# Kernel optimization log

Measured on AMD Instinct MI355X. Metric: run time of the kernel, lower is better.

Reference implementation:

```python
import jax, jax.numpy as jnp
import numpy as np

N_NODES = 50000


def setup_inputs() -> dict:
    key = jax.random.key(0)
    ks = jax.random.split(key, 8)
    x = jax.random.normal(ks[0], (N_NODES, 128), dtype=jnp.float32)
    edge_index = jax.random.randint(ks[1], (2, 800000), 0, N_NODES, dtype=jnp.int64)
    # Glorot-ish small init for weights
    W1l = jax.random.normal(ks[2], (128, 256), dtype=jnp.float32) * 0.05
    W1r = jax.random.normal(ks[3], (128, 256), dtype=jnp.float32) * 0.05
    b1 = jnp.zeros((256,), dtype=jnp.float32)
    W2l = jax.random.normal(ks[4], (256, 64), dtype=jnp.float32) * 0.05
    W2r = jax.random.normal(ks[5], (256, 64), dtype=jnp.float32) * 0.05
    b2 = jnp.zeros((64,), dtype=jnp.float32)
    return {"x": x, "edge_index": edge_index, "W1l": W1l, "W1r": W1r,
            "b1": b1, "W2l": W2l, "W2r": W2r, "b2": b2}


def _mean_aggregate(x, src, dst, num_nodes):
    # gather neighbor features [E, d], scatter-sum to targets, divide by in-degree
    summed = jax.ops.segment_sum(x[src], dst, num_segments=num_nodes)
    deg = jax.ops.segment_sum(jnp.ones_like(dst, dtype=x.dtype), dst,
                              num_segments=num_nodes)
    return summed / jnp.maximum(deg, 1.0)[:, None]


def _sage_conv(x, src, dst, W_l, W_r, b):
    # PyG SAGEConv (mean aggr): lin_l(mean_j x_j) + lin_r(x); bias only in lin_l
    agg = _mean_aggregate(x, src, dst, x.shape[0])
    return agg @ W_l + b + x @ W_r


def reference(x, edge_index, W1l, W1r, b1, W2l, W2r, b2):
    src, dst = edge_index[0], edge_index[1]
    h = jax.nn.relu(_sage_conv(x, src, dst, W1l, W1r, b1))
    # dropout p=0.5 is identity in eval mode
    out = _sage_conv(h, src, dst, W2l, W2r, b2)
    return out
```

## Files before the change

kernel.cpp:

```cpp
#include <hip/hip_runtime.h>
#include <hip/hip_bf16.h>

#define N_NODES 50000
#define CAP 64
#define NPART 8
#define PSZ 6250

typedef __attribute__((ext_vector_type(8))) __bf16 bf16x8;
typedef __attribute__((ext_vector_type(4))) float f32x4;

__device__ __forceinline__ unsigned short f2bf(float f) {
    union { float f; unsigned u; } c{f};
    unsigned u = c.u;
    return (unsigned short)((u + 0x7FFFu + ((u >> 16) & 1u)) >> 16);
}
__device__ __forceinline__ float bf2f(unsigned h) {
    union { unsigned u; float f; } c{h << 16};
    return c.f;
}
__device__ __forceinline__ unsigned pack2(float a, float b) {
    return (unsigned)f2bf(a) | ((unsigned)f2bf(b) << 16);
}

__device__ __forceinline__ unsigned q8(float v) {
    int q = __float2int_rn(v * 16.0f);
    q = max(-127, min(127, q));
    return (unsigned)(q + 128) & 0xFFu;
}

__global__ __launch_bounds__(256) void zero_kernel(uint4* __restrict__ p, int n4) {
    int i = blockIdx.x * 256 + threadIdx.x;
    if (i < n4) p[i] = (uint4){0u, 0u, 0u, 0u};
}

__global__ __launch_bounds__(256) void prep_all_kernel(
        const int* __restrict__ src, const int* __restrict__ dst,
        int* __restrict__ cnt, int* __restrict__ eidx, int E,
        const float4* __restrict__ x4, uint4* __restrict__ xb4,
        uint2* __restrict__ xq2, int NX,
        const float* __restrict__ W1l, const float* __restrict__ W1r,
        const float* __restrict__ W2l, const float* __restrict__ W2r,
        unsigned short* __restrict__ Wb1l, unsigned short* __restrict__ Wb1r,
        unsigned short* __restrict__ Wb2) {
    const int HB = (E + 1023) / 1024;
    const int CB = (NX + 255) / 256;
    int b = blockIdx.x;
    if (b < HB * NPART) {
        const int part = b & (NPART - 1);
        const int slice = b >> 3;
        const int lo = part * PSZ;
        int base = slice * 1024 + threadIdx.x;
#pragma unroll
        for (int k = 0; k < 4; ++k) {
            int e = base + k * 256;
            if (e < E) {
                int d = dst[e];
                if ((unsigned)(d - lo) < (unsigned)PSZ) {
                    int r = atomicAdd(&cnt[d], 1);
                    eidx[(size_t)d * CAP + (r & (CAP - 1))] = src[e];
                }
            }
        }
        return;
    }
    b -= HB * NPART;
    if (b < CB) {
        int t = b * 256 + threadIdx.x;
        if (t < NX) {
            float4 v0 = x4[2 * t];
            float4 v1 = x4[2 * t + 1];
            uint4 o;
            o.x = pack2(v0.x, v0.y);
            o.y = pack2(v0.z, v0.w);
            o.z = pack2(v1.x, v1.y);
            o.w = pack2(v1.z, v1.w);
            xb4[t] = o;
            uint2 q;
            q.x = q8(v0.x) | (q8(v0.y) << 8) | (q8(v0.z) << 16) | (q8(v0.w) << 24);
            q.y = q8(v1.x) | (q8(v1.y) << 8) | (q8(v1.z) << 16) | (q8(v1.w) << 24);
            xq2[t] = q;
        }
        return;
    }
    b -= CB;
    int t = b * 256 + threadIdx.x;
    if (t >= 12288) return;
    int g = t & 4095;
    int colin = g & 15;
    int rest = g >> 4;
    if (t < 4096) {
        int kb = rest & 15, cb = rest >> 4;
        int col = cb * 16 + colin;
#pragma unroll
        for (int j = 0; j < 8; ++j) Wb1l[g * 8 + j] = f2bf(W1l[(kb * 8 + j) * 256 + col]);
    } else if (t < 8192) {
        int kb = rest & 15, cb = rest >> 4;
        int col = cb * 16 + colin;
#pragma unroll
        for (int j = 0; j < 8; ++j) Wb1r[g * 8 + j] = f2bf(W1r[(kb * 8 + j) * 256 + col]);
    } else {
        int kb = rest & 31, cb = rest >> 5;
        const float* W = (cb < 4) ? W2l : W2r;
        int col = (cb < 4) ? (cb * 16 + colin) : ((cb - 4) * 16 + colin);
#pragma unroll
        for (int j = 0; j < 8; ++j) Wb2[g * 8 + j] = f2bf(W[(kb * 8 + j) * 64 + col]);
    }
}

__global__ __launch_bounds__(256) void agg1_kernel(const uint4* __restrict__ xq4,
        const int* __restrict__ cnt, const int* __restrict__ eidx,
        uint4* __restrict__ aggb4, int N) {
    int t = blockIdx.x * 256 + threadIdx.x;
    int n = t >> 6, lane = t & 63;
    if (n >= N) return;
    int deg = min(cnt[n], CAP);
    const int* el = eidx + (size_t)n * CAP;
    int g = lane >> 3, c = lane & 7;
    float s[16];
#pragma unroll
    for (int k = 0; k < 16; ++k) s[k] = 0.0f;
    for (int j = g; j < deg; j += 8) {
        int idx = el[j];
        uint4 v = xq4[(size_t)idx * 8 + c];
        unsigned w0 = v.x, w1 = v.y, w2 = v.z, w3 = v.w;
#pragma unroll
        for (int byte = 0; byte < 4; ++byte) {
            s[0 + byte]  += (float)((w0 >> (8 * byte)) & 0xFFu);
            s[4 + byte]  += (float)((w1 >> (8 * byte)) & 0xFFu);
            s[8 + byte]  += (float)((w2 >> (8 * byte)) & 0xFFu);
            s[12 + byte] += (float)((w3 >> (8 * byte)) & 0xFFu);
        }
    }
#pragma unroll
    for (int m = 8; m <= 32; m <<= 1) {
#pragma unroll
        for (int k = 0; k < 16; ++k) s[k] += __shfl_xor(s[k], m);
    }
    if (g == 0) {
        float scale = 0.0625f / (float)max(deg, 1);
        float bias = 128.0f * (float)deg;
        float v[16];
#pragma unroll
        for (int k = 0; k < 16; ++k) v[k] = (s[k] - bias) * scale;
        uint4 o0, o1;
        o0.x = pack2(v[0], v[1]);
        o0.y = pack2(v[2], v[3]);
        o0.z = pack2(v[4], v[5]);
        o0.w = pack2(v[6], v[7]);
        o1.x = pack2(v[8], v[9]);
        o1.y = pack2(v[10], v[11]);
        o1.z = pack2(v[12], v[13]);
        o1.w = pack2(v[14], v[15]);
        aggb4[(size_t)n * 16 + c * 2] = o0;
        aggb4[(size_t)n * 16 + c * 2 + 1] = o1;
    }
}

__global__ __launch_bounds__(256, 4) void gemm1_mfma(
        const unsigned short* __restrict__ xb, const unsigned short* __restrict__ aggb,
        const unsigned short* __restrict__ Wb1l, const unsigned short* __restrict__ Wb1r,
        const float* __restrict__ b1, unsigned short* __restrict__ hb, int M) {
    __shared__ uint4 wlds[2048];
    const int tid = threadIdx.x;
    const int wave = tid >> 6, lane = tid & 63;
    const int l16 = lane & 15, lq = lane >> 4;
    const int cg = blockIdx.y;
    const int base_row = blockIdx.x * 256 + wave * 64;
    int row_a[4];
#pragma unroll
    for (int rt = 0; rt < 4; ++rt) row_a[rt] = min(base_row + rt * 16 + l16, M - 1);

    const uint4* Wg1 = reinterpret_cast<const uint4*>(Wb1l) + cg * 1024;
    const uint4* Wg2 = reinterpret_cast<const uint4*>(Wb1r) + cg * 1024;
    for (int i = tid; i < 1024; i += 256) {
        wlds[i] = Wg1[i];
        wlds[1024 + i] = Wg2[i];
    }

    f32x4 acc[4][4];
#pragma unroll
    for (int rt = 0; rt < 4; ++rt)
#pragma unroll
        for (int q = 0; q < 4; ++q) acc[rt][q] = (f32x4){0.f, 0.f, 0.f, 0.f};

    __syncthreads();
#pragma unroll
    for (int s = 0; s < 2; ++s) {
        const unsigned short* A = (s == 0) ? aggb : xb;
        const uint4* wl = wlds + s * 1024;
#pragma unroll
        for (int ks = 0; ks < 4; ++ks) {
            bf16x8 a[4];
#pragma unroll
            for (int rt = 0; rt < 4; ++rt)
                a[rt] = *reinterpret_cast<const bf16x8*>(A + (size_t)row_a[rt] * 128 + ks * 32 + lq * 8);
            int wb = (ks * 4 + lq) * 16 + l16;
#pragma unroll
            for (int q = 0; q < 4; ++q) {
                bf16x8 bfr = *reinterpret_cast<const bf16x8*>(&wl[q * 256 + wb]);
#pragma unroll
                for (int rt = 0; rt < 4; ++rt)
                    acc[rt][q] = __builtin_amdgcn_mfma_f32_16x16x32_bf16(a[rt], bfr, acc[rt][q], 0, 0, 0);
            }
        }
    }

#pragma unroll
    for (int q = 0; q < 4; ++q) {
        int col = (cg * 4 + q) * 16 + l16;
        float bias = b1[col];
#pragma unroll
        for (int rt = 0; rt < 4; ++rt)
#pragma unroll
            for (int r = 0; r < 4; ++r) {
                int row = base_row + rt * 16 + lq * 4 + r;
                if (row < M) {
                    float v = acc[rt][q][r] + bias;
                    hb[(size_t)row * 256 + col] = f2bf(v > 0.0f ? v : 0.0f);
                }
            }
    }
}

__global__ __launch_bounds__(256, 4) void gemm2_mfma(
        const unsigned short* __restrict__ hb, const unsigned short* __restrict__ Wb2,
        unsigned short* __restrict__ tb, float* __restrict__ u, int M) {
    __shared__ uint4 wlds[2048];
    const int tid = threadIdx.x;
    const int wave = tid >> 6, lane = tid & 63;
    const int l16 = lane & 15, lq = lane >> 4;
    const int cg = blockIdx.y;
    const int base_row = blockIdx.x * 256 + wave * 64;
    int row_a[4];
#pragma unroll
    for (int rt = 0; rt < 4; ++rt) row_a[rt] = min(base_row + rt * 16 + l16, M - 1);

    const uint4* Wg = reinterpret_cast<const uint4*>(Wb2) + cg * 2048;
    for (int i = tid; i < 2048; i += 256) wlds[i] = Wg[i];

    f32x4 acc[4][4];
#pragma unroll
    for (int rt = 0; rt < 4; ++rt)
#pragma unroll
        for (int q = 0; q < 4; ++q) acc[rt][q] = (f32x4){0.f, 0.f, 0.f, 0.f};

    __syncthreads();
#pragma unroll
    for (int ks = 0; ks < 8; ++ks) {
        bf16x8 a[4];
#pragma unroll
        for (int rt = 0; rt < 4; ++rt)
            a[rt] = *reinterpret_cast<const bf16x8*>(hb + (size_t)row_a[rt] * 256 + ks * 32 + lq * 8);
        int wb = (ks * 4 + lq) * 16 + l16;
#pragma unroll
        for (int q = 0; q < 4; ++q) {
            bf16x8 bfr = *reinterpret_cast<const bf16x8*>(&wlds[q * 512 + wb]);
#pragma unroll
            for (int rt = 0; rt < 4; ++rt)
                acc[rt][q] = __builtin_amdgcn_mfma_f32_16x16x32_bf16(a[rt], bfr, acc[rt][q], 0, 0, 0);
        }
    }

#pragma unroll
    for (int q = 0; q < 4; ++q) {
        int cb = cg * 4 + q;
#pragma unroll
        for (int rt = 0; rt < 4; ++rt)
#pragma unroll
            for (int r = 0; r < 4; ++r) {
                int row = base_row + rt * 16 + lq * 4 + r;
                if (row >= M) continue;
                float v = acc[rt][q][r];
                if (cb < 4) tb[(size_t)row * 64 + cb * 16 + l16] = f2bf(v);
                else        u[(size_t)row * 64 + (cb - 4) * 16 + l16] = v;
            }
    }
}

__global__ __launch_bounds__(256) void agg2_kernel(const uint4* __restrict__ tb4,
        const float4* __restrict__ u4, const float4* __restrict__ b24,
        const int* __restrict__ cnt, const int* __restrict__ eidx,
        float4* __restrict__ out4, int N) {
    int t = blockIdx.x * 256 + threadIdx.x;
    int n = t >> 6, lane = t & 63;
    if (n >= N) return;
    int deg = min(cnt[n], CAP);
    const int* el = eidx + (size_t)n * CAP;
    int g = lane >> 3, c = lane & 7;
    float s0 = 0, s1 = 0, s2 = 0, s3 = 0, s4 = 0, s5 = 0, s6 = 0, s7 = 0;
    for (int j = g; j < deg; j += 8) {
        int idx = el[j];
        uint4 v = tb4[(size_t)idx * 8 + c];
        s0 += bf2f(v.x & 0xFFFF); s1 += bf2f(v.x >> 16);
        s2 += bf2f(v.y & 0xFFFF); s3 += bf2f(v.y >> 16);
        s4 += bf2f(v.z & 0xFFFF); s5 += bf2f(v.z >> 16);
        s6 += bf2f(v.w & 0xFFFF); s7 += bf2f(v.w >> 16);
    }
#pragma unroll
    for (int m = 8; m <= 32; m <<= 1) {
        s0 += __shfl_xor(s0, m); s1 += __shfl_xor(s1, m);
        s2 += __shfl_xor(s2, m); s3 += __shfl_xor(s3, m);
        s4 += __shfl_xor(s4, m); s5 += __shfl_xor(s5, m);
        s6 += __shfl_xor(s6, m); s7 += __shfl_xor(s7, m);
    }
    if (g == 0) {
        float rd = 1.0f / (float)max(deg, 1);
        float4 ua = u4[(size_t)n * 16 + c * 2];
        float4 ub = u4[(size_t)n * 16 + c * 2 + 1];
        float4 ba = b24[c * 2];
        float4 bb = b24[c * 2 + 1];
        float4 oa = {s0 * rd + ua.x + ba.x, s1 * rd + ua.y + ba.y,
                     s2 * rd + ua.z + ba.z, s3 * rd + ua.w + ba.w};
        float4 ob = {s4 * rd + ub.x + bb.x, s5 * rd + ub.y + bb.y,
                     s6 * rd + ub.z + bb.z, s7 * rd + ub.w + bb.w};
        out4[(size_t)n * 16 + c * 2] = oa;
        out4[(size_t)n * 16 + c * 2 + 1] = ob;
    }
}

extern "C" void kernel_launch(void* const* d_in, const int* in_sizes, int n_in,
                              void* d_out, int out_size, void* d_ws, size_t ws_size,
                              hipStream_t stream) {
    const float* x   = (const float*)d_in[0];
    const int*   ei  = (const int*)d_in[1];
    const float* W1l = (const float*)d_in[2];
    const float* W1r = (const float*)d_in[3];
    const float* b1  = (const float*)d_in[4];
    const float* W2l = (const float*)d_in[5];
    const float* W2r = (const float*)d_in[6];
    const float* b2  = (const float*)d_in[7];
    float* out = (float*)d_out;

    const int E = in_sizes[1] / 2;
    const int N = N_NODES;
    const int* src = ei;
    const int* dst = ei + E;
    const int HB = (E + 1023) / 1024;
    const int NX = N * 16;
    const int CB = (NX + 255) / 256;
    const int WB = 48;

    char* ws = (char*)d_ws;
    int* cnt  = (int*)(ws);
    int* eidx = (int*)(ws + 200000);
    size_t off = 200000 + (size_t)N * CAP * 4;
    off = (off + 15) & ~(size_t)15;
    unsigned short* xb   = (unsigned short*)(ws + off);  off += (size_t)N * 128 * 2;
    unsigned char*  xq   = (unsigned char*)(ws + off);   off += (size_t)N * 128;
    unsigned short* aggb = (unsigned short*)(ws + off);  off += (size_t)N * 128 * 2;
    unsigned short* hb   = (unsigned short*)(ws + off);  off += (size_t)N * 256 * 2;
    unsigned short* tb   = (unsigned short*)(ws + off);  off += (size_t)N * 64 * 2;
    float*          ubuf = (float*)(ws + off);           off += (size_t)N * 64 * 4;
    unsigned short* Wb1l = (unsigned short*)(ws + off);  off += 128 * 256 * 2;
    unsigned short* Wb1r = (unsigned short*)(ws + off);  off += 128 * 256 * 2;
    unsigned short* Wb2  = (unsigned short*)(ws + off);  off += 256 * 128 * 2;

    {
        int n4 = N / 4;
        zero_kernel<<<(n4 + 255) / 256, 256, 0, stream>>>((uint4*)cnt, n4);
    }

    prep_all_kernel<<<HB * NPART + CB + WB, 256, 0, stream>>>(
        src, dst, cnt, eidx, E, (const float4*)x, (uint4*)xb, (uint2*)xq, NX,
        W1l, W1r, W2l, W2r, Wb1l, Wb1r, Wb2);

    agg1_kernel<<<(N * 64 + 255) / 256, 256, 0, stream>>>((const uint4*)xq, cnt, eidx,
                                                          (uint4*)aggb, N);
    {
        dim3 grid((N + 255) / 256, 4);
        gemm1_mfma<<<grid, 256, 0, stream>>>(xb, aggb, Wb1l, Wb1r, b1, hb, N);
    }

    {
        dim3 grid((N + 255) / 256, 2);
        gemm2_mfma<<<grid, 256, 0, stream>>>(hb, Wb2, tb, ubuf, N);
    }
    agg2_kernel<<<(N * 64 + 255) / 256, 256, 0, stream>>>((const uint4*)tb, (const float4*)ubuf,
                                                          (const float4*)b2, cnt, eidx,
                                                          (float4*)out, N);
}
```

Measured before the change: 158.7 us.

## Fuse all stages into one cooperative persistent kernel with grid syncs

Replaces the six separate launches (zero, prep, agg1, gemm1, gemm2, agg2) with one cooperative kernel. It runs each stage as a grid-stride loop over virtual blocks, separated by grid.sync(). The grid is sized from the occupancy query and capped at 1024 blocks. This aims to remove per-launch overhead and inter-kernel gaps, at the cost of grid-wide barriers, fewer resident blocks for the memory-bound gather stages, and repeated LDS weight reloads per tile. The old multi-kernel path remains as a fallback if the cooperative launch fails.

```diff
diff --git a/kernel.cpp b/kernel.cpp
--- a/kernel.cpp
+++ b/kernel.cpp
@@ -1,5 +1,8 @@
 #include <hip/hip_runtime.h>
 #include <hip/hip_bf16.h>
+#include <hip/hip_cooperative_groups.h>
+
+namespace cg = cooperative_groups;
 
 #define N_NODES 50000
 #define CAP 64
@@ -21,11 +24,309 @@
 __device__ __forceinline__ unsigned pack2(float a, float b) {
     return (unsigned)f2bf(a) | ((unsigned)f2bf(b) << 16);
 }
-
-__device__ __forceinline__ unsigned q8(float v) {
+__device__ __forceinline__ unsigned q8x(float v) {
     int q = __float2int_rn(v * 16.0f);
     q = max(-127, min(127, q));
     return (unsigned)(q + 128) & 0xFFu;
+}
+
+struct Prm {
+    const int* src; const int* dst;
+    int* cnt; int* eidx; int E;
+    const float4* x4; uint4* xb4; uint2* xq2; int NX;
+    const float* W1l; const float* W1r; const float* W2l; const float* W2r;
+    unsigned short* Wb1l; unsigned short* Wb1r; unsigned short* Wb2;
+    const float* b1; unsigned short* hb;
+    unsigned short* tb; float* ubuf;
+    const float4* b24; float4* out4;
+    unsigned short* aggb;
+};
+
+__global__ __launch_bounds__(256, 4) void fused_kernel(Prm p) {
+    cg::grid_group grid = cg::this_grid();
+    __shared__ uint4 wlds[2048];
+    const int tid = threadIdx.x;
+    const int bid = blockIdx.x;
+    const int gsz = gridDim.x;
+
+    for (int i = bid * 256 + tid; i < N_NODES / 4; i += gsz * 256)
+        reinterpret_cast<uint4*>(p.cnt)[i] = (uint4){0u, 0u, 0u, 0u};
+    grid.sync();
+
+    {
+        const int HB = (p.E + 1023) / 1024;
+        const int HBP = HB * NPART;
+        const int CB = (p.NX + 255) / 256;
+        const int TOT = HBP + CB + 48;
+        for (int vb = bid; vb < TOT; vb += gsz) {
+            int b = vb;
+            if (b < HBP) {
+                const int part = b & (NPART - 1);
+                const int slice = b >> 3;
+                const int lo = part * PSZ;
+                int base = slice * 1024 + tid;
+#pragma unroll
+                for (int k = 0; k < 4; ++k) {
+                    int e = base + k * 256;
+                    if (e < p.E) {
+                        int d = p.dst[e];
+                        if ((unsigned)(d - lo) < (unsigned)PSZ) {
+                            int r = atomicAdd(&p.cnt[d], 1);
+                            p.eidx[(size_t)d * CAP + (r & (CAP - 1))] = p.src[e];
+                        }
+                    }
+                }
+                continue;
+            }
+            b -= HBP;
+            if (b < CB) {
+                int t = b * 256 + tid;
+                if (t < p.NX) {
+                    float4 v0 = p.x4[2 * t];
+                    float4 v1 = p.x4[2 * t + 1];
+                    uint4 o;
+                    o.x = pack2(v0.x, v0.y);
+                    o.y = pack2(v0.z, v0.w);
+                    o.z = pack2(v1.x, v1.y);
+                    o.w = pack2(v1.z, v1.w);
+                    p.xb4[t] = o;
+                    uint2 q;
+                    q.x = q8x(v0.x) | (q8x(v0.y) << 8) | (q8x(v0.z) << 16) | (q8x(v0.w) << 24);
+                    q.y = q8x(v1.x) | (q8x(v1.y) << 8) | (q8x(v1.z) << 16) | (q8x(v1.w) << 24);
+                    p.xq2[t] = q;
+                }
+                continue;
+            }
+            b -= CB;
+            int t = b * 256 + tid;
+            if (t >= 12288) continue;
+            int g = t & 4095;
+            int colin = g & 15;
+            int rest = g >> 4;
+            if (t < 4096) {
+                int kb = rest & 15, cb = rest >> 4;
+                int col = cb * 16 + colin;
+#pragma unroll
+                for (int j = 0; j < 8; ++j) p.Wb1l[g * 8 + j] = f2bf(p.W1l[(kb * 8 + j) * 256 + col]);
+            } else if (t < 8192) {
+                int kb = rest & 15, cb = rest >> 4;
+                int col = cb * 16 + colin;
+#pragma unroll
+                for (int j = 0; j < 8; ++j) p.Wb1r[g * 8 + j] = f2bf(p.W1r[(kb * 8 + j) * 256 + col]);
+            } else {
+                int kb = rest & 31, cb = rest >> 5;
+                const float* W = (cb < 4) ? p.W2l : p.W2r;
+                int col = (cb < 4) ? (cb * 16 + colin) : ((cb - 4) * 16 + colin);
+#pragma unroll
+                for (int j = 0; j < 8; ++j) p.Wb2[g * 8 + j] = f2bf(W[(kb * 8 + j) * 64 + col]);
+            }
+        }
+    }
+    grid.sync();
+
+    {
+        const uint4* xq4 = reinterpret_cast<const uint4*>(p.xq2);
+        uint4* aggb4 = reinterpret_cast<uint4*>(p.aggb);
+        for (int v = bid * 256 + tid; v < N_NODES * 64; v += gsz * 256) {
+            int n = v >> 6, lane = tid & 63;
+            int deg = min(p.cnt[n], CAP);
+            const int* el = p.eidx + (size_t)n * CAP;
+            int g = lane >> 3, c = lane & 7;
+            float s[16];
+#pragma unroll
+            for (int k = 0; k < 16; ++k) s[k] = 0.0f;
+            for (int j = g; j < deg; j += 8) {
+                int idx = el[j];
+                uint4 vv = xq4[(size_t)idx * 8 + c];
+                unsigned w0 = vv.x, w1 = vv.y, w2 = vv.z, w3 = vv.w;
+#pragma unroll
+                for (int byte = 0; byte < 4; ++byte) {
+                    s[0 + byte]  += (float)((w0 >> (8 * byte)) & 0xFFu);
+                    s[4 + byte]  += (float)((w1 >> (8 * byte)) & 0xFFu);
+                    s[8 + byte]  += (float)((w2 >> (8 * byte)) & 0xFFu);
+                    s[12 + byte] += (float)((w3 >> (8 * byte)) & 0xFFu);
+                }
+            }
+#pragma unroll
+            for (int m = 8; m <= 32; m <<= 1) {
+#pragma unroll
+                for (int k = 0; k < 16; ++k) s[k] += __shfl_xor(s[k], m);
+            }
+            if (g == 0) {
+                float scale = 0.0625f / (float)max(deg, 1);
+                float bias = 128.0f * (float)deg;
+                float vv[16];
+#pragma unroll
+                for (int k = 0; k < 16; ++k) vv[k] = (s[k] - bias) * scale;
+                uint4 o0, o1;
+                o0.x = pack2(vv[0], vv[1]);
+                o0.y = pack2(vv[2], vv[3]);
+                o0.z = pack2(vv[4], vv[5]);
+                o0.w = pack2(vv[6], vv[7]);
+                o1.x = pack2(vv[8], vv[9]);
+                o1.y = pack2(vv[10], vv[11]);
+                o1.z = pack2(vv[12], vv[13]);
+                o1.w = pack2(vv[14], vv[15]);
+                aggb4[(size_t)n * 16 + c * 2] = o0;
+                aggb4[(size_t)n * 16 + c * 2 + 1] = o1;
+            }
+        }
+    }
+    grid.sync();
+
+    {
+        const int wave = tid >> 6, lane = tid & 63;
+        const int l16 = lane & 15, lq = lane >> 4;
+        const int T1 = ((N_NODES + 255) / 256) * 4;
+        for (int vt = bid; vt < T1; vt += gsz) {
+            int bx = vt >> 2, cgq = vt & 3;
+            __syncthreads();
+            const uint4* Wg1 = reinterpret_cast<const uint4*>(p.Wb1l) + cgq * 1024;
+            const uint4* Wg2 = reinterpret_cast<const uint4*>(p.Wb1r) + cgq * 1024;
+            for (int i = tid; i < 1024; i += 256) {
+                wlds[i] = Wg1[i];
+                wlds[1024 + i] = Wg2[i];
+            }
+            const int base_row = bx * 256 + wave * 64;
+            int row_a[4];
+#pragma unroll
+            for (int rt = 0; rt < 4; ++rt) row_a[rt] = min(base_row + rt * 16 + l16, N_NODES - 1);
+            f32x4 acc[4][4];
+#pragma unroll
+            for (int rt = 0; rt < 4; ++rt)
+#pragma unroll
+                for (int q = 0; q < 4; ++q) acc[rt][q] = (f32x4){0.f, 0.f, 0.f, 0.f};
+            __syncthreads();
+#pragma unroll
+            for (int s = 0; s < 2; ++s) {
+                const unsigned short* A = (s == 0) ? p.aggb : reinterpret_cast<unsigned short*>(p.xb4);
+                const uint4* wl = wlds + s * 1024;
+#pragma unroll
+                for (int ks = 0; ks < 4; ++ks) {
+                    bf16x8 a[4];
+#pragma unroll
+                    for (int rt = 0; rt < 4; ++rt)
+                        a[rt] = *reinterpret_cast<const bf16x8*>(A + (size_t)row_a[rt] * 128 + ks * 32 + lq * 8);
+                    int wb = (ks * 4 + lq) * 16 + l16;
+#pragma unroll
+                    for (int q = 0; q < 4; ++q) {
+                        bf16x8 bfr = *reinterpret_cast<const bf16x8*>(&wl[q * 256 + wb]);
+#pragma unroll
+                        for (int rt = 0; rt < 4; ++rt)
+                            acc[rt][q] = __builtin_amdgcn_mfma_f32_16x16x32_bf16(a[rt], bfr, acc[rt][q], 0, 0, 0);
+                    }
+                }
+            }
+#pragma unroll
+            for (int q = 0; q < 4; ++q) {
+                int col = (cgq * 4 + q) * 16 + l16;
+                float bias = p.b1[col];
+#pragma unroll
+                for (int rt = 0; rt < 4; ++rt)
+#pragma unroll
+                    for (int r = 0; r < 4; ++r) {
+                        int row = base_row + rt * 16 + lq * 4 + r;
+                        if (row < N_NODES) {
+                            float v = acc[rt][q][r] + bias;
+                            p.hb[(size_t)row * 256 + col] = f2bf(v > 0.0f ? v : 0.0f);
+                        }
+                    }
+            }
+        }
+    }
+    grid.sync();
+
+    {
+        const int wave = tid >> 6, lane = tid & 63;
+        const int l16 = lane & 15, lq = lane >> 4;
+        const int T2 = ((N_NODES + 255) / 256) * 2;
+        for (int vt = bid; vt < T2; vt += gsz) {
+            int bx = vt >> 1, cgq = vt & 1;
+            __syncthreads();
+            const uint4* Wg = reinterpret_cast<const uint4*>(p.Wb2) + cgq * 2048;
+            for (int i = tid; i < 2048; i += 256) wlds[i] = Wg[i];
+            const int base_row = bx * 256 + wave * 64;
+            int row_a[4];
+#pragma unroll
+            for (int rt = 0; rt < 4; ++rt) row_a[rt] = min(base_row + rt * 16 + l16, N_NODES - 1);
+            f32x4 acc[4][4];
+#pragma unroll
+            for (int rt = 0; rt < 4; ++rt)
+#pragma unroll
+                for (int q = 0; q < 4; ++q) acc[rt][q] = (f32x4){0.f, 0.f, 0.f, 0.f};
+            __syncthreads();
+#pragma unroll
+            for (int ks = 0; ks < 8; ++ks) {
+                bf16x8 a[4];
+#pragma unroll
+                for (int rt = 0; rt < 4; ++rt)
+                    a[rt] = *reinterpret_cast<const bf16x8*>(p.hb + (size_t)row_a[rt] * 256 + ks * 32 + lq * 8);
+                int wb = (ks * 4 + lq) * 16 + l16;
+#pragma unroll
+                for (int q = 0; q < 4; ++q) {
+                    bf16x8 bfr = *reinterpret_cast<const bf16x8*>(&wlds[q * 512 + wb]);
+#pragma unroll
+                    for (int rt = 0; rt < 4; ++rt)
+                        acc[rt][q] = __builtin_amdgcn_mfma_f32_16x16x32_bf16(a[rt], bfr, acc[rt][q], 0, 0, 0);
+                }
+            }
+#pragma unroll
+            for (int q = 0; q < 4; ++q) {
+                int cb = cgq * 4 + q;
+#pragma unroll
+                for (int rt = 0; rt < 4; ++rt)
+#pragma unroll
+                    for (int r = 0; r < 4; ++r) {
+                        int row = base_row + rt * 16 + lq * 4 + r;
+                        if (row >= N_NODES) continue;
+                        float v = acc[rt][q][r];
+                        if (cb < 4) p.tb[(size_t)row * 64 + cb * 16 + l16] = f2bf(v);
+                        else        p.ubuf[(size_t)row * 64 + (cb - 4) * 16 + l16] = v;
+                    }
+            }
+        }
+    }
+    grid.sync();
+
+    {
+        const uint4* tb4 = reinterpret_cast<const uint4*>(p.tb);
+        const float4* u4 = reinterpret_cast<const float4*>(p.ubuf);
+        for (int v = bid * 256 + tid; v < N_NODES * 64; v += gsz * 256) {
+            int n = v >> 6, lane = tid & 63;
+            int deg = min(p.cnt[n], CAP);
+            const int* el = p.eidx + (size_t)n * CAP;
+            int g = lane >> 3, c = lane & 7;
+            float s0 = 0, s1 = 0, s2 = 0, s3 = 0, s4 = 0, s5 = 0, s6 = 0, s7 = 0;
+            for (int j = g; j < deg; j += 8) {
+                int idx = el[j];
+                uint4 vv = tb4[(size_t)idx * 8 + c];
+                s0 += bf2f(vv.x & 0xFFFF); s1 += bf2f(vv.x >> 16);
+                s2 += bf2f(vv.y & 0xFFFF); s3 += bf2f(vv.y >> 16);
+                s4 += bf2f(vv.z & 0xFFFF); s5 += bf2f(vv.z >> 16);
+                s6 += bf2f(vv.w & 0xFFFF); s7 += bf2f(vv.w >> 16);
+            }
+#pragma unroll
+            for (int m = 8; m <= 32; m <<= 1) {
+                s0 += __shfl_xor(s0, m); s1 += __shfl_xor(s1, m);
+                s2 += __shfl_xor(s2, m); s3 += __shfl_xor(s3, m);
+                s4 += __shfl_xor(s4, m); s5 += __shfl_xor(s5, m);
+                s6 += __shfl_xor(s6, m); s7 += __shfl_xor(s7, m);
+            }
+            if (g == 0) {
+                float rd = 1.0f / (float)max(deg, 1);
+                float4 ua = u4[(size_t)n * 16 + c * 2];
+                float4 ub = u4[(size_t)n * 16 + c * 2 + 1];
+                float4 ba = p.b24[c * 2];
+                float4 bb = p.b24[c * 2 + 1];
+                float4 oa = {s0 * rd + ua.x + ba.x, s1 * rd + ua.y + ba.y,
+                             s2 * rd + ua.z + ba.z, s3 * rd + ua.w + ba.w};
+                float4 ob = {s4 * rd + ub.x + bb.x, s5 * rd + ub.y + bb.y,
+                             s6 * rd + ub.z + bb.z, s7 * rd + ub.w + bb.w};
+                p.out4[(size_t)n * 16 + c * 2] = oa;
+                p.out4[(size_t)n * 16 + c * 2 + 1] = ob;
+            }
+        }
+    }
 }
 
 __global__ __launch_bounds__(256) void zero_kernel(uint4* __restrict__ p, int n4) {
@@ -76,8 +377,8 @@
             o.w = pack2(v1.z, v1.w);
             xb4[t] = o;
             uint2 q;
-            q.x = q8(v0.x) | (q8(v0.y) << 8) | (q8(v0.z) << 16) | (q8(v0.w) << 24);
-            q.y = q8(v1.x) | (q8(v1.y) << 8) | (q8(v1.z) << 16) | (q8(v1.w) << 24);
+            q.x = q8x(v0.x) | (q8x(v0.y) << 8) | (q8x(v0.z) << 16) | (q8x(v0.w) << 24);
+            q.y = q8x(v1.x) | (q8x(v1.y) << 8) | (q8x(v1.z) << 16) | (q8x(v1.w) << 24);
             xq2[t] = q;
         }
         return;
@@ -164,14 +465,14 @@
     const int tid = threadIdx.x;
     const int wave = tid >> 6, lane = tid & 63;
     const int l16 = lane & 15, lq = lane >> 4;
-    const int cg = blockIdx.y;
+    const int cgq = blockIdx.y;
     const int base_row = blockIdx.x * 256 + wave * 64;
     int row_a[4];
 #pragma unroll
     for (int rt = 0; rt < 4; ++rt) row_a[rt] = min(base_row + rt * 16 + l16, M - 1);
 
-    const uint4* Wg1 = reinterpret_cast<const uint4*>(Wb1l) + cg * 1024;
-    const uint4* Wg2 = reinterpret_cast<const uint4*>(Wb1r) + cg * 1024;
+    const uint4* Wg1 = reinterpret_cast<const uint4*>(Wb1l) + cgq * 1024;
+    const uint4* Wg2 = reinterpret_cast<const uint4*>(Wb1r) + cgq * 1024;
     for (int i = tid; i < 1024; i += 256) {
         wlds[i] = Wg1[i];
         wlds[1024 + i] = Wg2[i];
@@ -207,7 +508,7 @@
 
 #pragma unroll
     for (int q = 0; q < 4; ++q) {
-        int col = (cg * 4 + q) * 16 + l16;
+        int col = (cgq * 4 + q) * 16 + l16;
         float bias = b1[col];
 #pragma unroll
         for (int rt = 0; rt < 4; ++rt)
@@ -229,13 +530,13 @@
     const int tid = threadIdx.x;
     const int wave = tid >> 6, lane = tid & 63;
     const int l16 = lane & 15, lq = lane >> 4;
-    const int cg = blockIdx.y;
+    const int cgq = blockIdx.y;
     const int base_row = blockIdx.x * 256 + wave * 64;
     int row_a[4];
 #pragma unroll
     for (int rt = 0; rt < 4; ++rt) row_a[rt] = min(base_row + rt * 16 + l16, M - 1);
 
-    const uint4* Wg = reinterpret_cast<const uint4*>(Wb2) + cg * 2048;
+    const uint4* Wg = reinterpret_cast<const uint4*>(Wb2) + cgq * 2048;
     for (int i = tid; i < 2048; i += 256) wlds[i] = Wg[i];
 
     f32x4 acc[4][4];
@@ -263,7 +564,7 @@
 
 #pragma unroll
     for (int q = 0; q < 4; ++q) {
-        int cb = cg * 4 + q;
+        int cb = cgq * 4 + q;
 #pragma unroll
         for (int rt = 0; rt < 4; ++rt)
 #pragma unroll
@@ -333,12 +634,6 @@
 
     const int E = in_sizes[1] / 2;
     const int N = N_NODES;
-    const int* src = ei;
-    const int* dst = ei + E;
-    const int HB = (E + 1023) / 1024;
-    const int NX = N * 16;
-    const int CB = (NX + 255) / 256;
-    const int WB = 48;
 
     char* ws = (char*)d_ws;
     int* cnt  = (int*)(ws);
@@ -355,27 +650,60 @@
     unsigned short* Wb1r = (unsigned short*)(ws + off);  off += 128 * 256 * 2;
     unsigned short* Wb2  = (unsigned short*)(ws + off);  off += 256 * 128 * 2;
 
-    {
-        int n4 = N / 4;
-        zero_kernel<<<(n4 + 255) / 256, 256, 0, stream>>>((uint4*)cnt, n4);
-    }
-
-    prep_all_kernel<<<HB * NPART + CB + WB, 256, 0, stream>>>(
-        src, dst, cnt, eidx, E, (const float4*)x, (uint4*)xb, (uint2*)xq, NX,
-        W1l, W1r, W2l, W2r, Wb1l, Wb1r, Wb2);
-
-    agg1_kernel<<<(N * 64 + 255) / 256, 256, 0, stream>>>((const uint4*)xq, cnt, eidx,
-                                                          (uint4*)aggb, N);
-    {
-        dim3 grid((N + 255) / 256, 4);
-        gemm1_mfma<<<grid, 256, 0, stream>>>(xb, aggb, Wb1l, Wb1r, b1, hb, N);
-    }
-
-    {
-        dim3 grid((N + 255) / 256, 2);
-        gemm2_mfma<<<grid, 256, 0, stream>>>(hb, Wb2, tb, ubuf, N);
-    }
-    agg2_kernel<<<(N * 64 + 255) / 256, 256, 0, stream>>>((const uint4*)tb, (const float4*)ubuf,
-                                                          (const float4*)b2, cnt, eidx,
-                                                          (float4*)out, N);
-}
+    Prm prm;
+    prm.src = ei;
+    prm.dst = ei + E;
+    prm.cnt = cnt;
+    prm.eidx = eidx;
+    prm.E = E;
+    prm.x4 = (const float4*)x;
+    prm.xb4 = (uint4*)xb;
+    prm.xq2 = (uint2*)xq;
+    prm.NX = N * 16;
+    prm.W1l = W1l; prm.W1r = W1r; prm.W2l = W2l; prm.W2r = W2r;
+    prm.Wb1l = Wb1l; prm.Wb1r = Wb1r; prm.Wb2 = Wb2;
+    prm.b1 = b1; prm.hb = hb;
+    prm.tb = tb; prm.ubuf = ubuf;
+    prm.b24 = (const float4*)b2;
+    prm.out4 = (float4*)out;
+    prm.aggb = aggb;
+
+    bool done = false;
+    int blocksPerCU = 0;
+    hipError_t eq = hipOccupancyMaxActiveBlocksPerMultiprocessor(
+        &blocksPerCU, (const void*)fused_kernel, 256, 0);
+    if (eq == hipSuccess && blocksPerCU > 0) {
+        long long nblk = (long long)blocksPerCU * 256;
+        if (nblk > 1024) nblk = 1024;
+        nblk &= ~(long long)7;
+        if (nblk >= 8) {
+            void* args[] = {&prm};
+            hipError_t el = hipLaunchCooperativeKernel(
+                (const void*)fused_kernel, dim3((unsigned)nblk), dim3(256), args, 0, stream);
+            done = (el == hipSuccess);
+        }
+    }
+
+    if (!done) {
+        const int HB = (E + 1023) / 1024;
+        const int NX = N * 16;
+        const int CB = (NX + 255) / 256;
+        zero_kernel<<<(N / 4 + 255) / 256, 256, 0, stream>>>((uint4*)cnt, N / 4);
+        prep_all_kernel<<<HB * NPART + CB + 48, 256, 0, stream>>>(
+            ei, ei + E, cnt, eidx, E, (const float4*)x, (uint4*)xb, (uint2*)xq, NX,
+            W1l, W1r, W2l, W2r, Wb1l, Wb1r, Wb2);
+        agg1_kernel<<<(N * 64 + 255) / 256, 256, 0, stream>>>((const uint4*)xq, cnt, eidx,
+                                                              (uint4*)aggb, N);
+        {
+            dim3 grid((N + 255) / 256, 4);
+            gemm1_mfma<<<grid, 256, 0, stream>>>(xb, aggb, Wb1l, Wb1r, b1, hb, N);
+        }
+        {
+            dim3 grid((N + 255) / 256, 2);
+            gemm2_mfma<<<grid, 256, 0, stream>>>(hb, Wb2, tb, ubuf, N);
+        }
+        agg2_kernel<<<(N * 64 + 255) / 256, 256, 0, stream>>>((const uint4*)tb, (const float4*)ubuf,
+                                                              (const float4*)b2, cnt, eidx,
+                                                              (float4*)out, N);
+    }
+}
```

After: 547.9 us. 3.45x slower.
